# Optimization experiments

Hardware: AMD Instinct MI355X
Metric: run time of the kernel (lower is better)

The kernel has to match this reference:

```python
import jax, jax.numpy as jnp
import numpy as np

N_NODES = 100000
N_EDGES = 1600000
N_GRAPHS = 1000
D_IN = 128
HID = 128
OUT = 6


def setup_inputs() -> dict:
    key = jax.random.key(0)
    ks = jax.random.split(key, 12)
    s = 1.0 / np.sqrt(HID)
    x = jax.random.normal(ks[0], (N_NODES, D_IN), dtype=jnp.float32)
    ei = jax.random.randint(ks[1], (2, N_EDGES), 0, N_NODES, dtype=jnp.int64)
    batch = jnp.sort(jax.random.randint(ks[2], (N_NODES,), 0, N_GRAPHS, dtype=jnp.int64))
    return {
        "x": x,
        "ei": ei,
        "batch": batch,
        "W1a": jax.random.normal(ks[3], (D_IN, HID), dtype=jnp.float32) * s,
        "b1a": jnp.zeros((HID,), jnp.float32),
        "W1b": jax.random.normal(ks[4], (HID, HID), dtype=jnp.float32) * s,
        "b1b": jnp.zeros((HID,), jnp.float32),
        "W2a": jax.random.normal(ks[5], (HID, HID), dtype=jnp.float32) * s,
        "b2a": jnp.zeros((HID,), jnp.float32),
        "W2b": jax.random.normal(ks[6], (HID, HID), dtype=jnp.float32) * s,
        "b2b": jnp.zeros((HID,), jnp.float32),
        "Wlin": jax.random.normal(ks[7], (HID, OUT), dtype=jnp.float32) * s,
        "blin": jnp.zeros((OUT,), jnp.float32),
    }


def _gin_conv(x, src, dst, Wa, ba, Wb, bb):
    # PyG GINConv (eps=0): mlp(x_i + sum_{j->i} x_j)
    agg = jax.ops.segment_sum(x[src], dst, num_segments=N_NODES)
    h = agg + x
    h = jnp.maximum(h @ Wa + ba, 0.0)
    return h @ Wb + bb


def reference(x, ei, batch, W1a, b1a, W1b, b1b, W2a, b2a, W2b, b2b, Wlin, blin):
    src, dst = ei[0], ei[1]
    h = jnp.maximum(_gin_conv(x, src, dst, W1a, b1a, W1b, b1b), 0.0)
    # dropout is identity in eval mode
    h = _gin_conv(h, src, dst, W2a, b2a, W2b, b2b)
    # global mean pool per graph
    sums = jax.ops.segment_sum(h, batch, num_segments=N_GRAPHS)
    cnts = jax.ops.segment_sum(jnp.ones((h.shape[0], 1), h.dtype), batch, num_segments=N_GRAPHS)
    pooled = sums / jnp.maximum(cnts, 1.0)
    return pooled @ Wlin + blin
```

## Files before the change

### kernel.cpp

```cpp
#include <hip/hip_runtime.h>

#define N_NODES 100000
#define N_EDGES 1600000
#define N_GRAPHS 1000
#define HID 128
#define OUTD 6

#define BUCK_LOG 7
#define BUCK_W (1 << BUCK_LOG)
#define NBUCK ((N_NODES + BUCK_W - 1) >> BUCK_LOG)
#define BCAP 4096
#define FILL_BLOCKS 512
#define FILL_CHUNK 3128

#define CVT_BLOCKS 6250
#define GST_BLOCKS 391
#define PACK_BLOCKS 32
#define PREP_BLOCKS (CVT_BLOCKS + GST_BLOCKS + PACK_BLOCKS + FILL_BLOCKS)

typedef _Float16 h2 __attribute__((ext_vector_type(2)));
typedef _Float16 half8 __attribute__((ext_vector_type(8)));
typedef float f32x4 __attribute__((ext_vector_type(4)));

__global__ __launch_bounds__(256) void k_prep(const float* __restrict__ x,
                                              const int* __restrict__ batch,
                                              const int* __restrict__ srcv,
                                              const int* __restrict__ dstv,
                                              const float* __restrict__ W1a,
                                              const float* __restrict__ W1b,
                                              const float* __restrict__ W2a,
                                              const float* __restrict__ W2b,
                                              _Float16* __restrict__ X16,
                                              int* __restrict__ gstart,
                                              _Float16* __restrict__ P,
                                              int* __restrict__ bcur0,
                                              int* __restrict__ packed) {
    __shared__ int h[NBUCK];
    __shared__ int lcur[NBUCK];
    int b = blockIdx.x, t = threadIdx.x;
    if (b < FILL_BLOCKS) {
        int e0 = b * FILL_CHUNK;
        int e1 = min(e0 + FILL_CHUNK, N_EDGES);
        for (int i = t; i < NBUCK; i += 256) h[i] = 0;
        __syncthreads();
        int ev = e0 + ((e1 - e0) & ~3);
        for (int e = e0 + t * 4; e < ev; e += 1024) {
            int4 d4 = *(const int4*)(dstv + e);
            atomicAdd(&h[d4.x >> BUCK_LOG], 1);
            atomicAdd(&h[d4.y >> BUCK_LOG], 1);
            atomicAdd(&h[d4.z >> BUCK_LOG], 1);
            atomicAdd(&h[d4.w >> BUCK_LOG], 1);
        }
        for (int e = ev + t; e < e1; e += 256) atomicAdd(&h[dstv[e] >> BUCK_LOG], 1);
        __syncthreads();
        for (int i = t; i < NBUCK; i += 256) {
            int c = h[i];
            lcur[i] = c ? atomicAdd(&bcur0[i], c) : 0;
        }
        __syncthreads();
        for (int e = e0 + t * 4; e < ev; e += 1024) {
            int4 d4 = *(const int4*)(dstv + e);
            int4 s4 = *(const int4*)(srcv + e);
            int b0 = d4.x >> BUCK_LOG, b1 = d4.y >> BUCK_LOG;
            int b2 = d4.z >> BUCK_LOG, b3 = d4.w >> BUCK_LOG;
            int p0 = atomicAdd(&lcur[b0], 1);
            int p1 = atomicAdd(&lcur[b1], 1);
            int p2 = atomicAdd(&lcur[b2], 1);
            int p3 = atomicAdd(&lcur[b3], 1);
            if (p0 < BCAP) packed[b0 * BCAP + p0] = ((d4.x & (BUCK_W - 1)) << 20) | s4.x;
            if (p1 < BCAP) packed[b1 * BCAP + p1] = ((d4.y & (BUCK_W - 1)) << 20) | s4.y;
            if (p2 < BCAP) packed[b2 * BCAP + p2] = ((d4.z & (BUCK_W - 1)) << 20) | s4.z;
            if (p3 < BCAP) packed[b3 * BCAP + p3] = ((d4.w & (BUCK_W - 1)) << 20) | s4.w;
        }
        for (int e = ev + t; e < e1; e += 256) {
            int d = dstv[e];
            int bk = d >> BUCK_LOG;
            int pos = atomicAdd(&lcur[bk], 1);
            if (pos < BCAP) packed[bk * BCAP + pos] = ((d & (BUCK_W - 1)) << 20) | srcv[e];
        }
    } else if (b < FILL_BLOCKS + CVT_BLOCKS) {
        size_t i = ((size_t)(b - FILL_BLOCKS) * 256 + t) * 8;
        float4 v0 = *(const float4*)(x + i);
        float4 v1 = *(const float4*)(x + i + 4);
        half8 o;
        o[0] = (_Float16)v0.x; o[1] = (_Float16)v0.y; o[2] = (_Float16)v0.z; o[3] = (_Float16)v0.w;
        o[4] = (_Float16)v1.x; o[5] = (_Float16)v1.y; o[6] = (_Float16)v1.z; o[7] = (_Float16)v1.w;
        *(half8*)(X16 + i) = o;
    } else if (b < FILL_BLOCKS + CVT_BLOCKS + GST_BLOCKS) {
        int n = (b - FILL_BLOCKS - CVT_BLOCKS) * 256 + t;
        if (n < N_NODES) {
            int bb = batch[n];
            int prev = (n == 0) ? -1 : batch[n - 1];
            for (int g = prev + 1; g <= bb; ++g) gstart[g] = n;
            if (n == N_NODES - 1)
                for (int g = bb + 1; g <= N_GRAPHS; ++g) gstart[g] = N_NODES;
        }
    } else {
        int gid = (b - FILL_BLOCKS - CVT_BLOCKS - GST_BLOCKS) * 256 + t;
        int mat = gid >> 11;
        int r = gid & 2047;
        int ctks = r >> 6;
        int lane = r & 63;
        int col = (ctks >> 2) * 16 + (lane & 15);
        int k0 = (ctks & 3) * 32 + (lane >> 4) * 8;
        const float* W = (mat == 0) ? W1a : (mat == 1) ? W1b : (mat == 2) ? W2a : W2b;
        _Float16* dp = P + mat * 16384 + r * 8;
#pragma unroll
        for (int j = 0; j < 8; ++j) dp[j] = (_Float16)W[(k0 + j) * HID + col];
    }
}

__global__ __launch_bounds__(256) void k_csrfine(const int* __restrict__ packed,
                                                 const int* __restrict__ bcur0,
                                                 int* __restrict__ offsets,
                                                 int* __restrict__ csr_src) {
    __shared__ int hist[BUCK_W];
    __shared__ int scan[BUCK_W];
    __shared__ int cur[BUCK_W];
    __shared__ int red[4];
    int b = blockIdx.x;
    int base = b << BUCK_LOG;
    int t = threadIdx.x;
    int partial = 0;
    for (int j = t; j < b; j += 256) partial += bcur0[j];
#pragma unroll
    for (int d = 32; d > 0; d >>= 1) partial += __shfl_down(partial, d, 64);
    if ((t & 63) == 0) red[t >> 6] = partial;
    __syncthreads();
    int s = red[0] + red[1] + red[2] + red[3];
    int cnt = bcur0[b];
    const int* pb = packed + b * BCAP;

    if (t < BUCK_W) hist[t] = 0;
    __syncthreads();
    for (int i = t; i < cnt; i += 256) atomicAdd(&hist[pb[i] >> 20], 1);
    __syncthreads();
    if (t < BUCK_W) scan[t] = hist[t];
    __syncthreads();
    for (int d = 1; d < BUCK_W; d <<= 1) {
        int a = 0;
        if (t >= d && t < BUCK_W) a = scan[t - d];
        __syncthreads();
        if (t < BUCK_W) scan[t] += a;
        __syncthreads();
    }
    if (t < BUCK_W) {
        int node = base + t;
        if (node < N_NODES) {
            int excl = scan[t] - hist[t];
            offsets[node] = s + excl;
            cur[t] = excl;
        }
    }
    if (b == 0 && t == 0) offsets[N_NODES] = N_EDGES;
    __syncthreads();
    for (int i = t; i < cnt; i += 256) {
        int v = pb[i];
        int ln = v >> 20;
        int pos = atomicAdd(&cur[ln], 1);
        csr_src[s + pos] = v & 0xFFFFF;
    }
}

__global__ __launch_bounds__(256) void k_gather16(const _Float16* __restrict__ x,
                                                  const int* __restrict__ csr,
                                                  const int* __restrict__ offs,
                                                  _Float16* __restrict__ out) {
    int t = threadIdx.x;
    int wave = t >> 6, lane = t & 63;
    int g = lane >> 4;
    int l = lane & 15;
    int node = blockIdx.x * 16 + wave * 4 + g;
    const half8* xp8 = (const half8*)x;
    int s = offs[node], e = offs[node + 1];
    int cnt = e - s;
    int mx = cnt;
#pragma unroll
    for (int d = 32; d > 0; d >>= 1) mx = max(mx, __shfl_xor(mx, d, 64));

    half8 acc0 = xp8[(size_t)node * 16 + l];
    half8 acc1 = {0, 0, 0, 0, 0, 0, 0, 0};

    for (int it = 0; it < mx; it += 4) {
        int p = s + it;
        int i0 = -1, i1 = -1, i2 = -1, i3 = -1;
        if (p + 0 < e) i0 = csr[p + 0];
        if (p + 1 < e) i1 = csr[p + 1];
        if (p + 2 < e) i2 = csr[p + 2];
        if (p + 3 < e) i3 = csr[p + 3];
        if (i0 >= 0) acc0 += xp8[(size_t)i0 * 16 + l];
        if (i1 >= 0) acc1 += xp8[(size_t)i1 * 16 + l];
        if (i2 >= 0) acc0 += xp8[(size_t)i2 * 16 + l];
        if (i3 >= 0) acc1 += xp8[(size_t)i3 * 16 + l];
    }
    ((half8*)out)[(size_t)node * 16 + l] = acc0 + acc1;
}

static __device__ __forceinline__ unsigned long long pack4(float v0, float v1,
                                                           float v2, float v3) {
    union { h2 h[2]; unsigned long long u; } u;
    h2 p0, p1;
    p0[0] = (_Float16)v0; p0[1] = (_Float16)v1;
    p1[0] = (_Float16)v2; p1[1] = (_Float16)v3;
    u.h[0] = p0; u.h[1] = p1;
    return u.u;
}

template <int RELU_OUT>
__global__ __launch_bounds__(256, 2) void k_mlp16(const _Float16* __restrict__ in,
                                                  const _Float16* __restrict__ Wap,
                                                  const float* __restrict__ ba,
                                                  const _Float16* __restrict__ Wbp,
                                                  const float* __restrict__ bb,
                                                  _Float16* __restrict__ out) {
    __shared__ uint4 WaS4[2048];
    __shared__ uint4 WbS4[2048];
    __shared__ unsigned long long hS[4][512];
    int t = threadIdx.x;
    int wave = t >> 6, lane = t & 63;
    int l = lane & 15, w = lane >> 4;
    int row0 = blockIdx.x * 256 + wave * 64;

    const uint4* wa4 = (const uint4*)Wap;
    const uint4* wb4 = (const uint4*)Wbp;
#pragma unroll
    for (int i = 0; i < 8; ++i) WaS4[t + i * 256] = wa4[t + i * 256];
#pragma unroll
    for (int i = 0; i < 8; ++i) WbS4[t + i * 256] = wb4[t + i * 256];
    __syncthreads();
    const half8* waf = (const half8*)WaS4;
    const half8* wbf = (const half8*)WbS4;
    unsigned long long* h64 = hS[wave];
    int swz = ((l & 3) << 2) ^ (((l >> 2) & 1) << 1);

    float4 baR[8], bbR[8];
#pragma unroll
    for (int ct = 0; ct < 8; ++ct) {
        baR[ct] = *(const float4*)(ba + ct * 16 + w * 4);
        bbR[ct] = *(const float4*)(bb + ct * 16 + w * 4);
    }

#pragma unroll
    for (int tile = 0; tile < 4; ++tile) {
        int row = row0 + tile * 16 + l;
        bool rok = row < N_NODES;
        const _Float16* rp = in + (size_t)row * HID + w * 8;
        half8 xf[4];
#pragma unroll
        for (int ks = 0; ks < 4; ++ks) {
            half8 v = {0, 0, 0, 0, 0, 0, 0, 0};
            if (rok) v = *(const half8*)(rp + ks * 32);
            xf[ks] = v;
        }
#pragma unroll
        for (int ct = 0; ct < 8; ++ct) {
            f32x4 c = {0.f, 0.f, 0.f, 0.f};
#pragma unroll
            for (int ks = 0; ks < 4; ++ks)
                c = __builtin_amdgcn_mfma_f32_16x16x32_f16(waf[(ct * 4 + ks) * 64 + lane],
                                                           xf[ks], c, 0, 0, 0);
            float4 b4 = baR[ct];
            h64[l * 32 + ((ct * 4 + w) ^ swz)] =
                pack4(fmaxf(c[0] + b4.x, 0.f), fmaxf(c[1] + b4.y, 0.f),
                      fmaxf(c[2] + b4.z, 0.f), fmaxf(c[3] + b4.w, 0.f));
        }
        half8 hf[4];
#pragma unroll
        for (int ks = 0; ks < 4; ++ks) {
            int slot = (ks * 8 + w * 2) ^ swz;
            hf[ks] = *(const half8*)&h64[l * 32 + slot];
        }
#pragma unroll
        for (int ct = 0; ct < 8; ++ct) {
            f32x4 c = {0.f, 0.f, 0.f, 0.f};
#pragma unroll
            for (int ks = 0; ks < 4; ++ks)
                c = __builtin_amdgcn_mfma_f32_16x16x32_f16(wbf[(ct * 4 + ks) * 64 + lane],
                                                           hf[ks], c, 0, 0, 0);
            float4 b4 = bbR[ct];
            float v0 = c[0] + b4.x, v1 = c[1] + b4.y, v2 = c[2] + b4.z, v3 = c[3] + b4.w;
            if (RELU_OUT) {
                v0 = fmaxf(v0, 0.f); v1 = fmaxf(v1, 0.f);
                v2 = fmaxf(v2, 0.f); v3 = fmaxf(v3, 0.f);
            }
            if (rok)
                *(unsigned long long*)(out + (size_t)row * HID + ct * 16 + w * 4) =
                    pack4(v0, v1, v2, v3);
        }
    }
}

__global__ __launch_bounds__(256) void k_pool_head(const _Float16* __restrict__ h,
                                                   const int* __restrict__ gstart,
                                                   const float* __restrict__ Wlin,
                                                   const float* __restrict__ blin,
                                                   float* __restrict__ out) {
    __shared__ float sums[4][HID];
    int g = blockIdx.x;
    int t = threadIdx.x;
    int wave = t >> 6, lane = t & 63;
    int s = gstart[g], e = gstart[g + 1];
    float ax = 0.f, ay = 0.f;
    const h2* hp = (const h2*)h;
    int r = s + wave;
    for (; r + 12 < e; r += 16) {
        h2 v0 = hp[(size_t)r * 64 + lane];
        h2 v1 = hp[(size_t)(r + 4) * 64 + lane];
        h2 v2 = hp[(size_t)(r + 8) * 64 + lane];
        h2 v3 = hp[(size_t)(r + 12) * 64 + lane];
        ax += (float)v0[0] + (float)v1[0] + (float)v2[0] + (float)v3[0];
        ay += (float)v0[1] + (float)v1[1] + (float)v2[1] + (float)v3[1];
    }
    for (; r < e; r += 4) {
        h2 v = hp[(size_t)r * 64 + lane];
        ax += (float)v[0];
        ay += (float)v[1];
    }
    sums[wave][2 * lane] = ax;
    sums[wave][2 * lane + 1] = ay;
    __syncthreads();
    if (wave != 0) return;
    float c = fmaxf((float)(e - s), 1.0f);
    float px = (sums[0][2 * lane] + sums[1][2 * lane] + sums[2][2 * lane] + sums[3][2 * lane]) / c;
    float py = (sums[0][2 * lane + 1] + sums[1][2 * lane + 1] + sums[2][2 * lane + 1] +
                sums[3][2 * lane + 1]) / c;
#pragma unroll
    for (int o = 0; o < OUTD; ++o) {
        float v = px * Wlin[(2 * lane) * OUTD + o] + py * Wlin[(2 * lane + 1) * OUTD + o];
#pragma unroll
        for (int d = 32; d > 0; d >>= 1) v += __shfl_down(v, d, 64);
        if (lane == 0) out[g * OUTD + o] = v + blin[o];
    }
}

extern "C" void kernel_launch(void* const* d_in, const int* in_sizes, int n_in,
                              void* d_out, int out_size, void* d_ws, size_t ws_size,
                              hipStream_t stream) {
    const float* x    = (const float*)d_in[0];
    const int*   ei   = (const int*)d_in[1];
    const int*   batch= (const int*)d_in[2];
    const float* W1a  = (const float*)d_in[3];
    const float* b1a  = (const float*)d_in[4];
    const float* W1b  = (const float*)d_in[5];
    const float* b1b  = (const float*)d_in[6];
    const float* W2a  = (const float*)d_in[7];
    const float* b2a  = (const float*)d_in[8];
    const float* W2b  = (const float*)d_in[9];
    const float* b2b  = (const float*)d_in[10];
    const float* Wlin = (const float*)d_in[11];
    const float* blin = (const float*)d_in[12];
    const int* src = ei;
    const int* dst = ei + N_EDGES;
    float* out = (float*)d_out;

    char* ws = (char*)d_ws;
    size_t off = 0;
    auto alloc = [&](size_t bytes) -> void* {
        void* p = ws + off;
        off += (bytes + 255) & ~(size_t)255;
        return p;
    };
    _Float16* X16 = (_Float16*)alloc(2ull * N_NODES * HID);
    _Float16* M   = (_Float16*)alloc(2ull * N_NODES * HID + 65536);
    _Float16* H1  = (_Float16*)alloc(2ull * N_NODES * HID + 65536);
    int*   csr_src = (int*)alloc(sizeof(int) * (size_t)N_EDGES);
    int*   offsets = (int*)alloc(sizeof(int) * (N_NODES + 1));
    int*   gstart  = (int*)alloc(sizeof(int) * (N_GRAPHS + 1));
    int*   bcur0   = (int*)alloc(sizeof(int) * NBUCK);
    _Float16* Wpack = (_Float16*)alloc(2ull * 4 * 16384);
    int* packed = (int*)H1;
    _Float16* M2 = M;
    _Float16* H2 = X16;
    (void)ws_size; (void)in_sizes; (void)n_in; (void)out_size;

    hipMemsetAsync(bcur0, 0, sizeof(int) * NBUCK, stream);

    k_prep<<<PREP_BLOCKS, 256, 0, stream>>>(x, batch, src, dst, W1a, W1b, W2a, W2b,
                                            X16, gstart, Wpack, bcur0, packed);
    k_csrfine<<<NBUCK, 256, 0, stream>>>(packed, bcur0, offsets, csr_src);

    k_gather16<<<N_NODES / 16, 256, 0, stream>>>(X16, csr_src, offsets, M);
    k_mlp16<1><<<(N_NODES + 255) / 256, 256, 0, stream>>>(M, Wpack + 0 * 16384, b1a,
                                                          Wpack + 1 * 16384, b1b, H1);
    k_gather16<<<N_NODES / 16, 256, 0, stream>>>(H1, csr_src, offsets, M2);
    k_mlp16<0><<<(N_NODES + 255) / 256, 256, 0, stream>>>(M2, Wpack + 2 * 16384, b2a,
                                                          Wpack + 3 * 16384, b2b, H2);

    k_pool_head<<<N_GRAPHS, 256, 0, stream>>>(H2, gstart, Wlin, blin, out);
}
```

Before: 324.0 us.

## Assign one wavefront per node in gather with coalesced index load and shuffle reduction

The gather kernel now maps a whole 64-lane wave to one node instead of four nodes per wave. Neighbor indices are loaded coalesced, one per lane, and broadcast with shuffles, so four 16-lane groups each fetch a different neighbor row at once. Partial sums are then reduced across the groups with xor shuffles. This removes the per-wave max-degree divergence and the serial scalar index loads, at the cost of four times as many blocks and extra shuffle work.

```diff
diff --git a/kernel.cpp b/kernel.cpp
--- a/kernel.cpp
+++ b/kernel.cpp
@@ -162,6 +162,14 @@
     }
 }
 
+static __device__ __forceinline__ half8 shfl_xor_h8(half8 v, int mask) {
+    union { half8 h; int i[4]; } a, b;
+    a.h = v;
+#pragma unroll
+    for (int k = 0; k < 4; ++k) b.i[k] = __shfl_xor(a.i[k], mask, 64);
+    return b.h;
+}
+
 __global__ __launch_bounds__(256) void k_gather16(const _Float16* __restrict__ x,
                                                   const int* __restrict__ csr,
                                                   const int* __restrict__ offs,
@@ -170,30 +178,39 @@
     int wave = t >> 6, lane = t & 63;
     int g = lane >> 4;
     int l = lane & 15;
-    int node = blockIdx.x * 16 + wave * 4 + g;
+    int node = __builtin_amdgcn_readfirstlane(blockIdx.x * 4 + wave);
     const half8* xp8 = (const half8*)x;
     int s = offs[node], e = offs[node + 1];
-    int cnt = e - s;
-    int mx = cnt;
-#pragma unroll
-    for (int d = 32; d > 0; d >>= 1) mx = max(mx, __shfl_xor(mx, d, 64));
-
-    half8 acc0 = xp8[(size_t)node * 16 + l];
-    half8 acc1 = {0, 0, 0, 0, 0, 0, 0, 0};
-
-    for (int it = 0; it < mx; it += 4) {
-        int p = s + it;
-        int i0 = -1, i1 = -1, i2 = -1, i3 = -1;
-        if (p + 0 < e) i0 = csr[p + 0];
-        if (p + 1 < e) i1 = csr[p + 1];
-        if (p + 2 < e) i2 = csr[p + 2];
-        if (p + 3 < e) i3 = csr[p + 3];
-        if (i0 >= 0) acc0 += xp8[(size_t)i0 * 16 + l];
-        if (i1 >= 0) acc1 += xp8[(size_t)i1 * 16 + l];
-        if (i2 >= 0) acc0 += xp8[(size_t)i2 * 16 + l];
-        if (i3 >= 0) acc1 += xp8[(size_t)i3 * 16 + l];
-    }
-    ((half8*)out)[(size_t)node * 16 + l] = acc0 + acc1;
+
+    half8 z = {0, 0, 0, 0, 0, 0, 0, 0};
+    half8 acc0 = (g == 0) ? xp8[(size_t)node * 16 + l] : z;
+    half8 acc1 = z;
+
+    for (int base = s; base < e; base += 64) {
+        int cnt = e - base;
+        if (cnt > 64) cnt = 64;
+        int myidx = (base + lane < e) ? csr[base + lane] : 0;
+        int j = 0;
+        for (; j + 16 <= cnt; j += 16) {
+            int i0 = __shfl(myidx, j + g, 64);
+            int i1 = __shfl(myidx, j + 4 + g, 64);
+            int i2 = __shfl(myidx, j + 8 + g, 64);
+            int i3 = __shfl(myidx, j + 12 + g, 64);
+            acc0 += xp8[(size_t)i0 * 16 + l];
+            acc1 += xp8[(size_t)i1 * 16 + l];
+            acc0 += xp8[(size_t)i2 * 16 + l];
+            acc1 += xp8[(size_t)i3 * 16 + l];
+        }
+        for (; j < cnt; j += 4) {
+            int sl = j + g;
+            int idx = __shfl(myidx, sl < cnt ? sl : 0, 64);
+            if (sl < cnt) acc0 += xp8[(size_t)idx * 16 + l];
+        }
+    }
+    half8 r = acc0 + acc1;
+    r += shfl_xor_h8(r, 16);
+    r += shfl_xor_h8(r, 32);
+    if (g == 0) ((half8*)out)[(size_t)node * 16 + l] = r;
 }
 
 static __device__ __forceinline__ unsigned long long pack4(float v0, float v1,
@@ -379,10 +396,10 @@
                                             X16, gstart, Wpack, bcur0, packed);
     k_csrfine<<<NBUCK, 256, 0, stream>>>(packed, bcur0, offsets, csr_src);
 
-    k_gather16<<<N_NODES / 16, 256, 0, stream>>>(X16, csr_src, offsets, M);
+    k_gather16<<<N_NODES / 4, 256, 0, stream>>>(X16, csr_src, offsets, M);
     k_mlp16<1><<<(N_NODES + 255) / 256, 256, 0, stream>>>(M, Wpack + 0 * 16384, b1a,
                                                           Wpack + 1 * 16384, b1b, H1);
-    k_gather16<<<N_NODES / 16, 256, 0, stream>>>(H1, csr_src, offsets, M2);
+    k_gather16<<<N_NODES / 4, 256, 0, stream>>>(H1, csr_src, offsets, M2);
     k_mlp16<0><<<(N_NODES + 255) / 256, 256, 0, stream>>>(M2, Wpack + 2 * 16384, b2a,
                                                           Wpack + 3 * 16384, b2b, H2);
 
```

Result: faster. 312.6 us (-3.5%).

## Fuse neighbor gather into MLP kernel to drop aggregated intermediate buffer

Applied to the files above, without the earlier changes.

The separate gather kernel is removed and each GIN layer's neighbor sum is computed inside the MLP kernel. Each lane accumulates its row's neighbors straight into the MFMA input fragments, so the aggregated tensor is never written to global memory and read back. The cost is a different gather pattern: each 16-lane group now walks the edges of 16 different rows, with divergent trip counts up to the wave maximum and scattered 16-byte loads. The MLP kernel also runs only about 2 blocks per CU with large shared memory, so it may hide gather latency less well. The packed edge buffer gets its own allocation because H1 can no longer be aliased.

```diff
diff --git a/kernel.cpp b/kernel.cpp
--- a/kernel.cpp
+++ b/kernel.cpp
@@ -162,40 +162,6 @@
     }
 }
 
-__global__ __launch_bounds__(256) void k_gather16(const _Float16* __restrict__ x,
-                                                  const int* __restrict__ csr,
-                                                  const int* __restrict__ offs,
-                                                  _Float16* __restrict__ out) {
-    int t = threadIdx.x;
-    int wave = t >> 6, lane = t & 63;
-    int g = lane >> 4;
-    int l = lane & 15;
-    int node = blockIdx.x * 16 + wave * 4 + g;
-    const half8* xp8 = (const half8*)x;
-    int s = offs[node], e = offs[node + 1];
-    int cnt = e - s;
-    int mx = cnt;
-#pragma unroll
-    for (int d = 32; d > 0; d >>= 1) mx = max(mx, __shfl_xor(mx, d, 64));
-
-    half8 acc0 = xp8[(size_t)node * 16 + l];
-    half8 acc1 = {0, 0, 0, 0, 0, 0, 0, 0};
-
-    for (int it = 0; it < mx; it += 4) {
-        int p = s + it;
-        int i0 = -1, i1 = -1, i2 = -1, i3 = -1;
-        if (p + 0 < e) i0 = csr[p + 0];
-        if (p + 1 < e) i1 = csr[p + 1];
-        if (p + 2 < e) i2 = csr[p + 2];
-        if (p + 3 < e) i3 = csr[p + 3];
-        if (i0 >= 0) acc0 += xp8[(size_t)i0 * 16 + l];
-        if (i1 >= 0) acc1 += xp8[(size_t)i1 * 16 + l];
-        if (i2 >= 0) acc0 += xp8[(size_t)i2 * 16 + l];
-        if (i3 >= 0) acc1 += xp8[(size_t)i3 * 16 + l];
-    }
-    ((half8*)out)[(size_t)node * 16 + l] = acc0 + acc1;
-}
-
 static __device__ __forceinline__ unsigned long long pack4(float v0, float v1,
                                                            float v2, float v3) {
     union { h2 h[2]; unsigned long long u; } u;
@@ -207,12 +173,14 @@
 }
 
 template <int RELU_OUT>
-__global__ __launch_bounds__(256, 2) void k_mlp16(const _Float16* __restrict__ in,
-                                                  const _Float16* __restrict__ Wap,
-                                                  const float* __restrict__ ba,
-                                                  const _Float16* __restrict__ Wbp,
-                                                  const float* __restrict__ bb,
-                                                  _Float16* __restrict__ out) {
+__global__ __launch_bounds__(256, 2) void k_gmlp(const _Float16* __restrict__ x,
+                                                 const int* __restrict__ csr,
+                                                 const int* __restrict__ offs,
+                                                 const _Float16* __restrict__ Wap,
+                                                 const float* __restrict__ ba,
+                                                 const _Float16* __restrict__ Wbp,
+                                                 const float* __restrict__ bb,
+                                                 _Float16* __restrict__ out) {
     __shared__ uint4 WaS4[2048];
     __shared__ uint4 WbS4[2048];
     __shared__ unsigned long long hS[4][512];
@@ -240,18 +208,59 @@
         bbR[ct] = *(const float4*)(bb + ct * 16 + w * 4);
     }
 
+    const half8* xp8 = (const half8*)x;
+
 #pragma unroll
     for (int tile = 0; tile < 4; ++tile) {
         int row = row0 + tile * 16 + l;
         bool rok = row < N_NODES;
-        const _Float16* rp = in + (size_t)row * HID + w * 8;
+        int s = 0, e = 0;
+        if (rok) { s = offs[row]; e = offs[row + 1]; }
+        int deg = e - s;
+        int mx = deg;
+#pragma unroll
+        for (int d = 32; d > 0; d >>= 1) mx = max(mx, __shfl_xor(mx, d, 64));
+
+        half8 z = {0, 0, 0, 0, 0, 0, 0, 0};
         half8 xf[4];
 #pragma unroll
         for (int ks = 0; ks < 4; ++ks) {
-            half8 v = {0, 0, 0, 0, 0, 0, 0, 0};
-            if (rok) v = *(const half8*)(rp + ks * 32);
+            half8 v = z;
+            if (rok) v = xp8[(size_t)row * 16 + w + ks * 4];
             xf[ks] = v;
         }
+        half8 g0 = z, g1 = z, g2 = z, g3 = z;
+        int j = 0;
+        for (; j + 2 <= mx; j += 2) {
+            int i0 = (j < deg) ? csr[s + j] : -1;
+            int i1 = (j + 1 < deg) ? csr[s + j + 1] : -1;
+            if (i0 >= 0) {
+                size_t b0 = (size_t)i0 * 16 + w;
+                xf[0] += xp8[b0];
+                xf[1] += xp8[b0 + 4];
+                xf[2] += xp8[b0 + 8];
+                xf[3] += xp8[b0 + 12];
+            }
+            if (i1 >= 0) {
+                size_t b1 = (size_t)i1 * 16 + w;
+                g0 += xp8[b1];
+                g1 += xp8[b1 + 4];
+                g2 += xp8[b1 + 8];
+                g3 += xp8[b1 + 12];
+            }
+        }
+        if (j < mx) {
+            int i0 = (j < deg) ? csr[s + j] : -1;
+            if (i0 >= 0) {
+                size_t b0 = (size_t)i0 * 16 + w;
+                xf[0] += xp8[b0];
+                xf[1] += xp8[b0 + 4];
+                xf[2] += xp8[b0 + 8];
+                xf[3] += xp8[b0 + 12];
+            }
+        }
+        xf[0] += g0; xf[1] += g1; xf[2] += g2; xf[3] += g3;
+
 #pragma unroll
         for (int ct = 0; ct < 8; ++ct) {
             f32x4 c = {0.f, 0.f, 0.f, 0.f};
@@ -361,15 +370,13 @@
         return p;
     };
     _Float16* X16 = (_Float16*)alloc(2ull * N_NODES * HID);
-    _Float16* M   = (_Float16*)alloc(2ull * N_NODES * HID + 65536);
     _Float16* H1  = (_Float16*)alloc(2ull * N_NODES * HID + 65536);
     int*   csr_src = (int*)alloc(sizeof(int) * (size_t)N_EDGES);
     int*   offsets = (int*)alloc(sizeof(int) * (N_NODES + 1));
     int*   gstart  = (int*)alloc(sizeof(int) * (N_GRAPHS + 1));
     int*   bcur0   = (int*)alloc(sizeof(int) * NBUCK);
     _Float16* Wpack = (_Float16*)alloc(2ull * 4 * 16384);
-    int* packed = (int*)H1;
-    _Float16* M2 = M;
+    int* packed = (int*)alloc(sizeof(int) * (size_t)NBUCK * BCAP);
     _Float16* H2 = X16;
     (void)ws_size; (void)in_sizes; (void)n_in; (void)out_size;
 
@@ -379,12 +386,12 @@
                                             X16, gstart, Wpack, bcur0, packed);
     k_csrfine<<<NBUCK, 256, 0, stream>>>(packed, bcur0, offsets, csr_src);
 
-    k_gather16<<<N_NODES / 16, 256, 0, stream>>>(X16, csr_src, offsets, M);
-    k_mlp16<1><<<(N_NODES + 255) / 256, 256, 0, stream>>>(M, Wpack + 0 * 16384, b1a,
-                                                          Wpack + 1 * 16384, b1b, H1);
-    k_gather16<<<N_NODES / 16, 256, 0, stream>>>(H1, csr_src, offsets, M2);
-    k_mlp16<0><<<(N_NODES + 255) / 256, 256, 0, stream>>>(M2, Wpack + 2 * 16384, b2a,
-                                                          Wpack + 3 * 16384, b2b, H2);
+    k_gmlp<1><<<(N_NODES + 255) / 256, 256, 0, stream>>>(X16, csr_src, offsets,
+                                                         Wpack + 0 * 16384, b1a,
+                                                         Wpack + 1 * 16384, b1b, H1);
+    k_gmlp<0><<<(N_NODES + 255) / 256, 256, 0, stream>>>(H1, csr_src, offsets,
+                                                         Wpack + 2 * 16384, b2a,
+                                                         Wpack + 3 * 16384, b2b, H2);
 
     k_pool_head<<<N_GRAPHS, 256, 0, stream>>>(H2, gstart, Wlin, blin, out);
 }
```

New measurement: 343.6 us. 1.06x slower.
